# Optimization experiments

Measured on AMD Instinct MI355X. Metric: run time of the kernel, lower is better.

The kernel has to match this reference:

```python
import jax, jax.numpy as jnp
import numpy as np

T = 8192
D = 2048

def setup_inputs() -> dict:
    key = jax.random.key(0)
    ks = jax.random.split(key, 8)
    s = 1.0 / np.sqrt(D)
    return {
        "x": jax.random.normal(ks[0], (1, T, D), dtype=jnp.float32),
        "h0": jax.random.normal(ks[1], (1, D), dtype=jnp.float32),
        "W1": jax.random.uniform(ks[2], (D, D), jnp.float32, -s, s),
        "b1": jax.random.uniform(ks[3], (D,), jnp.float32, -s, s),
        "W2": jax.random.uniform(ks[4], (D, D), jnp.float32, -s, s),
        "b2": jax.random.uniform(ks[5], (D,), jnp.float32, -s, s),
        "Wf": jax.random.uniform(ks[6], (4, D), jnp.float32, -s, s),
        "bf": jax.random.uniform(ks[7], (4,), jnp.float32, -s, s),
    }

def reference(x, h0, W1, b1, W2, b2, Wf, bf):
    xs = x[0]                          # (T, D) -- squeeze(0)
    # fc1(x_i) has no recurrent dependency: precompute as one big GEMM (same math)
    pre = xs @ W1.T + b1               # (T, D)
    def step(h, p):
        # h: (1, D); p: (D,) broadcasts over the batch-of-1 row
        h = jax.nn.relu(p + h @ W2.T + b2)
        return h, None
    h, _ = jax.lax.scan(step, h0, pre)
    return h @ Wf.T + bf               # (1, 4)
```

## Files before the change

### kernel.cpp

```cpp
#include <hip/hip_runtime.h>

#define TT 8192
#define DD 2048
#define NWG 128
#define RPW 16
#define NTH 256
#define NREP 8

typedef unsigned long long u64;
#define SIGN2 0x8000000080000000ULL

#define BM 128
#define BN 128
#define BK 16

__global__ __launch_bounds__(NTH)
void gemm_abt_bias(const float* __restrict__ A, const float* __restrict__ B,
                   const float* __restrict__ bias, float* __restrict__ C,
                   int M, int N, int K) {
  __shared__ float As[BK][BM + 4];
  __shared__ float Bs[BK][BN + 4];
  const int ntile = N / BN;
  const int bn = blockIdx.x % ntile;
  const int bm = blockIdx.x / ntile;
  const int tid = (int)threadIdx.x;
  const int tx = tid & 15;
  const int ty = tid >> 4;

  float acc[8][8];
#pragma unroll
  for (int i = 0; i < 8; ++i)
#pragma unroll
    for (int j = 0; j < 8; ++j) acc[i][j] = 0.f;

  for (int kt = 0; kt < K; kt += BK) {
#pragma unroll
    for (int i = 0; i < 2; ++i) {
      int f = tid + i * 256;
      int row = f >> 2, c4 = f & 3;
      const float4 av = *(const float4*)(A + (size_t)(bm * BM + row) * K + kt + c4 * 4);
      As[c4 * 4 + 0][row] = av.x; As[c4 * 4 + 1][row] = av.y;
      As[c4 * 4 + 2][row] = av.z; As[c4 * 4 + 3][row] = av.w;
      const float4 bv = *(const float4*)(B + (size_t)(bn * BN + row) * K + kt + c4 * 4);
      Bs[c4 * 4 + 0][row] = bv.x; Bs[c4 * 4 + 1][row] = bv.y;
      Bs[c4 * 4 + 2][row] = bv.z; Bs[c4 * 4 + 3][row] = bv.w;
    }
    __syncthreads();
#pragma unroll
    for (int kk = 0; kk < BK; ++kk) {
      float a[8], b[8];
      *(float4*)&a[0] = *(const float4*)&As[kk][ty * 8];
      *(float4*)&a[4] = *(const float4*)&As[kk][ty * 8 + 4];
      *(float4*)&b[0] = *(const float4*)&Bs[kk][tx * 8];
      *(float4*)&b[4] = *(const float4*)&Bs[kk][tx * 8 + 4];
#pragma unroll
      for (int i = 0; i < 8; ++i)
#pragma unroll
        for (int j = 0; j < 8; ++j) acc[i][j] += a[i] * b[j];
    }
    __syncthreads();
  }

  const int col0 = bn * BN + tx * 8;
  const float4 bv0 = *(const float4*)(bias + col0);
  const float4 bv1 = *(const float4*)(bias + col0 + 4);
#pragma unroll
  for (int i = 0; i < 8; ++i) {
    float* crow = C + (size_t)(bm * BM + ty * 8 + i) * N + col0;
    float4 v0 = { acc[i][0] + bv0.x, acc[i][1] + bv0.y, acc[i][2] + bv0.z, acc[i][3] + bv0.w };
    float4 v1 = { acc[i][4] + bv1.x, acc[i][5] + bv1.y, acc[i][6] + bv1.z, acc[i][7] + bv1.w };
    *(float4*)(crow) = v0;
    *(float4*)(crow + 4) = v1;
  }
}

__device__ __forceinline__ float wave_sum(float v) {
#pragma unroll
  for (int off = 32; off > 0; off >>= 1) v += __shfl_down(v, off, 64);
  return v;
}

__device__ __forceinline__ u64 aload(const u64* p) {
  return __hip_atomic_load(p, __ATOMIC_RELAXED, __HIP_MEMORY_SCOPE_AGENT);
}
__device__ __forceinline__ void astore(u64* p, u64 v) {
  __hip_atomic_store(p, v, __ATOMIC_RELAXED, __HIP_MEMORY_SCOPE_AGENT);
}

__global__ void __launch_bounds__(NTH, 1)
recurrent_kernel(const float* __restrict__ h0,
                 const float* __restrict__ W2,
                 const float* __restrict__ b2,
                 const float* __restrict__ pre,
                 const float* __restrict__ Wf,
                 const float* __restrict__ bf,
                 float* __restrict__ out,
                 float* hbuf) {
  __shared__ float partial[2][4][RPW];
  __shared__ float hs[DD];

  const int wg   = (int)blockIdx.x;
  const int tid  = (int)threadIdx.x;
  const int lane = tid & 63;
  const int wave = tid >> 6;
  const int grp  = wg & (NREP - 1);
  const int k0   = 8 * tid;

  const int lp = ((lane & 1) << 3) | ((lane & 2) << 1) |
                 ((lane & 4) >> 1) | ((lane & 8) >> 3);

  float w2[RPW * 8];
#pragma unroll
  for (int j = 0; j < RPW; ++j) {
    const size_t r = (size_t)(wg * RPW + (j ^ lp));
    *(float4*)&w2[j * 8]     = *(const float4*)(W2 + r * DD + k0);
    *(float4*)&w2[j * 8 + 4] = *(const float4*)(W2 + r * DD + k0 + 4);
  }
#pragma unroll
  for (int i = 0; i < RPW * 8; i += 4)
    asm volatile("" : "+v"(w2[i]), "+v"(w2[i + 1]), "+v"(w2[i + 2]), "+v"(w2[i + 3]));

  float b2a = 0.f, b2b = 0.f;
  if (tid < 64) {
    const int c = tid >> 3;
    b2a = b2[wg * RPW + 2 * c];
    b2b = b2[wg * RPW + 2 * c + 1];
  }

  u64* const hbU = (u64*)hbuf;

  for (int t = 0; t < TT; ++t) {
    float2 p2 = {0.f, 0.f};
    if (tid < 64) p2 = *(const float2*)(pre + (size_t)t * DD + wg * RPW + 2 * (tid >> 3));

    float h[8];
    if (t == 0) {
      const float4 a = *(const float4*)(h0 + k0);
      const float4 b = *(const float4*)(h0 + k0 + 4);
      h[0]=a.x; h[1]=a.y; h[2]=a.z; h[3]=a.w;
      h[4]=b.x; h[5]=b.y; h[6]=b.z; h[7]=b.w;
    } else {
      u64* src = hbU + (size_t)((t & 1) * NREP + grp) * (DD / 2) + 4 * tid;
      const u64 EXP = ((t >> 1) & 1) ? SIGN2 : 0ULL;
      u64 u0, u1, u2, u3;
      for (;;) {
        u0 = aload(src + 0); u1 = aload(src + 1);
        u2 = aload(src + 2); u3 = aload(src + 3);
        if (((((u0 ^ EXP) | (u1 ^ EXP)) | ((u2 ^ EXP) | (u3 ^ EXP))) & SIGN2) == 0ULL)
          break;
        __builtin_amdgcn_s_sleep(1);
      }
      u0 &= ~SIGN2; u1 &= ~SIGN2; u2 &= ~SIGN2; u3 &= ~SIGN2;
      h[0]=__uint_as_float((unsigned)u0); h[1]=__uint_as_float((unsigned)(u0>>32));
      h[2]=__uint_as_float((unsigned)u1); h[3]=__uint_as_float((unsigned)(u1>>32));
      h[4]=__uint_as_float((unsigned)u2); h[5]=__uint_as_float((unsigned)(u2>>32));
      h[6]=__uint_as_float((unsigned)u3); h[7]=__uint_as_float((unsigned)(u3>>32));
    }

    float acc[RPW];
#pragma unroll
    for (int r = 0; r < RPW; ++r) acc[r] = 0.f;
#pragma unroll
    for (int i = 0; i < 8; ++i)
#pragma unroll
      for (int r = 0; r < RPW; ++r) acc[r] += w2[r * 8 + i] * h[i];

#pragma unroll
    for (int j = 0; j < 8; ++j) acc[j] += __shfl_xor(acc[8 + j], 1, 64);
#pragma unroll
    for (int j = 0; j < 4; ++j) acc[j] += __shfl_xor(acc[4 + j], 2, 64);
#pragma unroll
    for (int j = 0; j < 2; ++j) acc[j] += __shfl_xor(acc[2 + j], 4, 64);
    acc[0] += __shfl_xor(acc[1], 8, 64);
    acc[0] += __shfl_xor(acc[0], 16, 64);
    acc[0] += __shfl_xor(acc[0], 32, 64);

    if (lane < 16) partial[t & 1][wave][lp] = acc[0];
    __syncthreads();

    if (tid < 64) {
      const int c = tid >> 3, rp = tid & 7;
      const float* P = &partial[t & 1][0][0];
      const float s0 = P[0*RPW+2*c] + P[1*RPW+2*c] + P[2*RPW+2*c] + P[3*RPW+2*c];
      const float s1 = P[0*RPW+2*c+1] + P[1*RPW+2*c+1] + P[2*RPW+2*c+1] + P[3*RPW+2*c+1];
      const float v0 = fmaxf(p2.x + b2a + s0, 0.f);
      const float v1 = fmaxf(p2.y + b2b + s1, 0.f);
      u64 u = (((u64)__float_as_uint(v1) << 32) | (u64)__float_as_uint(v0)) & ~SIGN2;
      if (((t + 1) >> 1) & 1) u |= SIGN2;
      astore(hbU + (size_t)(((t + 1) & 1) * NREP + rp) * (DD / 2) + wg * 8 + c, u);
    }
  }

  if (wg != 0) return;

  {
    u64* src = hbU + 4 * tid;
    u64 u0, u1, u2, u3;
    for (;;) {
      u0 = aload(src + 0); u1 = aload(src + 1);
      u2 = aload(src + 2); u3 = aload(src + 3);
      if ((((u0 | u1) | (u2 | u3)) & SIGN2) == 0ULL) break;
      __builtin_amdgcn_s_sleep(1);
    }
    u64* dst = (u64*)hs + 4 * tid;
    dst[0] = u0; dst[1] = u1; dst[2] = u2; dst[3] = u3;
  }
  __syncthreads();
  float acc = 0.f;
#pragma unroll
  for (int j = 0; j < 8; ++j) {
    const float4 wv = *(const float4*)(Wf + (size_t)wave * DD + j * 256 + 4 * lane);
    const float4 hv = *(const float4*)&hs[j * 256 + 4 * lane];
    acc += wv.x * hv.x + wv.y * hv.y + wv.z * hv.z + wv.w * hv.w;
  }
  acc = wave_sum(acc);
  if (lane == 0) out[wave] = acc + bf[wave];
}

extern "C" void kernel_launch(void* const* d_in, const int* in_sizes, int n_in,
                              void* d_out, int out_size, void* d_ws, size_t ws_size,
                              hipStream_t stream) {
  const float* x  = (const float*)d_in[0];
  const float* h0 = (const float*)d_in[1];
  const float* W1 = (const float*)d_in[2];
  const float* b1 = (const float*)d_in[3];
  const float* W2 = (const float*)d_in[4];
  const float* b2 = (const float*)d_in[5];
  const float* Wf = (const float*)d_in[6];
  const float* bf = (const float*)d_in[7];
  float* out = (float*)d_out;

  float* pre  = (float*)d_ws;
  float* hbuf = pre + (size_t)TT * DD;

  hipMemsetAsync(hbuf, 0x00, NREP * DD * sizeof(float), stream);
  hipMemsetAsync(hbuf + NREP * DD, 0xAA, NREP * DD * sizeof(float), stream);

  gemm_abt_bias<<<dim3((TT / BM) * (DD / BN)), dim3(NTH), 0, stream>>>(
      x, W1, b1, pre, TT, DD, DD);
  recurrent_kernel<<<dim3(NWG), dim3(NTH), 0, stream>>>(
      h0, W2, b2, pre, Wf, bf, out, hbuf);
}
```

Measured before the change: 17.78 ms.

## Replace per-step block barrier with last-arriver LDS counter reduction

Removes the per-timestep __syncthreads in the recurrent kernel. Each wave bumps a shared-memory counter, and the last wave to arrive reduces the four partial sums, applies bias and ReLU, and publishes h with 32-bit atomic stores across all 64 lanes (two stores each for the 8 replicas). This lets early waves move on to polling the next step instead of waiting at a barrier, and spreads the stores across more lanes. It relies on LDS visibility ordering between waves without a barrier, which risks a race on partial and scnt reuse across parities.

```diff
diff --git a/kernel.cpp b/kernel.cpp
--- a/kernel.cpp
+++ b/kernel.cpp
@@ -8,7 +8,9 @@
 #define NREP 8
 
 typedef unsigned long long u64;
+typedef unsigned int u32;
 #define SIGN2 0x8000000080000000ULL
+#define SIGN1 0x80000000u
 
 #define BM 128
 #define BN 128
@@ -83,7 +85,7 @@
 __device__ __forceinline__ u64 aload(const u64* p) {
   return __hip_atomic_load(p, __ATOMIC_RELAXED, __HIP_MEMORY_SCOPE_AGENT);
 }
-__device__ __forceinline__ void astore(u64* p, u64 v) {
+__device__ __forceinline__ void astore32(u32* p, u32 v) {
   __hip_atomic_store(p, v, __ATOMIC_RELAXED, __HIP_MEMORY_SCOPE_AGENT);
 }
 
@@ -97,6 +99,7 @@
                  float* __restrict__ out,
                  float* hbuf) {
   __shared__ float partial[2][4][RPW];
+  __shared__ int   scnt[2];
   __shared__ float hs[DD];
 
   const int wg   = (int)blockIdx.x;
@@ -120,18 +123,17 @@
   for (int i = 0; i < RPW * 8; i += 4)
     asm volatile("" : "+v"(w2[i]), "+v"(w2[i + 1]), "+v"(w2[i + 2]), "+v"(w2[i + 3]));
 
-  float b2a = 0.f, b2b = 0.f;
-  if (tid < 64) {
-    const int c = tid >> 3;
-    b2a = b2[wg * RPW + 2 * c];
-    b2b = b2[wg * RPW + 2 * c + 1];
-  }
+  const int crow = wg * RPW + (lane & 15);
+  const float b2v = b2[crow];
+
+  if (tid == 0) { scnt[0] = 0; scnt[1] = 0; }
+  __syncthreads();
 
   u64* const hbU = (u64*)hbuf;
 
   for (int t = 0; t < TT; ++t) {
-    float2 p2 = {0.f, 0.f};
-    if (tid < 64) p2 = *(const float2*)(pre + (size_t)t * DD + wg * RPW + 2 * (tid >> 3));
+    const int par = t & 1;
+    const float preh = pre[(size_t)t * DD + crow];
 
     float h[8];
     if (t == 0) {
@@ -140,7 +142,7 @@
       h[0]=a.x; h[1]=a.y; h[2]=a.z; h[3]=a.w;
       h[4]=b.x; h[5]=b.y; h[6]=b.z; h[7]=b.w;
     } else {
-      u64* src = hbU + (size_t)((t & 1) * NREP + grp) * (DD / 2) + 4 * tid;
+      u64* src = hbU + (size_t)(par * NREP + grp) * (DD / 2) + 4 * tid;
       const u64 EXP = ((t >> 1) & 1) ? SIGN2 : 0ULL;
       u64 u0, u1, u2, u3;
       for (;;) {
@@ -175,19 +177,26 @@
     acc[0] += __shfl_xor(acc[0], 16, 64);
     acc[0] += __shfl_xor(acc[0], 32, 64);
 
-    if (lane < 16) partial[t & 1][wave][lp] = acc[0];
-    __syncthreads();
-
-    if (tid < 64) {
-      const int c = tid >> 3, rp = tid & 7;
-      const float* P = &partial[t & 1][0][0];
-      const float s0 = P[0*RPW+2*c] + P[1*RPW+2*c] + P[2*RPW+2*c] + P[3*RPW+2*c];
-      const float s1 = P[0*RPW+2*c+1] + P[1*RPW+2*c+1] + P[2*RPW+2*c+1] + P[3*RPW+2*c+1];
-      const float v0 = fmaxf(p2.x + b2a + s0, 0.f);
-      const float v1 = fmaxf(p2.y + b2b + s1, 0.f);
-      u64 u = (((u64)__float_as_uint(v1) << 32) | (u64)__float_as_uint(v0)) & ~SIGN2;
-      if (((t + 1) >> 1) & 1) u |= SIGN2;
-      astore(hbU + (size_t)(((t + 1) & 1) * NREP + rp) * (DD / 2) + wg * 8 + c, u);
+    if (lane < 16) partial[par][wave][lp] = acc[0];
+    asm volatile("s_waitcnt lgkmcnt(0)" ::: "memory");
+    int old = 0;
+    if (lane == 0) old = atomicAdd(&scnt[par], 1);
+    old = __shfl(old, 0, 64);
+
+    if (old == 3) {
+      asm volatile("" ::: "memory");
+      float v = partial[par][lane >> 4][lane & 15];
+      v += __shfl_xor(v, 16, 64);
+      v += __shfl_xor(v, 32, 64);
+      if (lane == 0) scnt[par] = 0;
+      asm volatile("s_waitcnt lgkmcnt(0)" ::: "memory");
+      const float r = fmaxf(v + preh + b2v, 0.f);
+      u32 bits = __float_as_uint(r);
+      if (((t + 1) >> 1) & 1) bits |= SIGN1;
+      const int slot8 = ((t + 1) & 1) * NREP;
+      u32* b0 = (u32*)hbuf + (size_t)(slot8 + (lane >> 4)) * DD + crow;
+      astore32(b0, bits);
+      astore32(b0 + 4 * DD, bits);
     }
   }
 
```

Measured after the change: 18.32 ms. 3.1% more time.
